# Kernel optimization log

Hardware: AMD Instinct MI355X
Metric: run time of the kernel (lower is better)

Reference implementation:

```python
import jax, jax.numpy as jnp
import numpy as np

B, T, D, H = 2, 2048, 1024, 16
HD = D // H  # head_dim = 64


def setup_inputs() -> dict:
    key = jax.random.key(0)
    k1, k2, k3 = jax.random.split(key, 3)
    s = 0.02
    return {
        "x": jax.random.normal(k1, (B, T, D), dtype=jnp.float32),
        "Wqkv": jax.random.normal(k2, (D, 3 * D), dtype=jnp.float32) * s,
        "bqkv": jnp.zeros((3 * D,), dtype=jnp.float32),
        "Wout": jax.random.normal(k3, (D, D), dtype=jnp.float32) * s,
        "bout": jnp.zeros((D,), dtype=jnp.float32),
    }


def reference(x, Wqkv, bqkv, Wout, bout):
    Bx, Tx, Dx = x.shape
    qkv = x @ Wqkv + bqkv                                  # [B,T,3D]
    qkv = qkv.reshape(Bx, Tx, 3, H, HD)
    q, k, v = (jnp.moveaxis(qkv, 2, 0)[i] for i in range(3))  # each [B,T,H,HD]
    q = q.transpose(0, 2, 1, 3)  # [B,H,T,HD]
    k = k.transpose(0, 2, 1, 3)
    v = v.transpose(0, 2, 1, 3)
    scale = 1.0 / jnp.sqrt(jnp.float32(HD))
    attn = jnp.einsum("bhqd,bhkd->bhqk", q, k) * scale     # [B,H,T,T]
    causal = jnp.tril(jnp.ones((Tx, Tx), dtype=bool))
    attn = jnp.where(causal, attn, -jnp.inf)
    attn = jax.nn.softmax(attn, axis=-1)
    out = jnp.einsum("bhqk,bhkd->bhqd", attn, v)           # [B,H,T,HD]
    out = out.transpose(0, 2, 1, 3).reshape(Bx, Tx, Dx)
    return out @ Wout + bout
```

## Files before the change

kernel.cpp:

```cpp
#include <hip/hip_runtime.h>
#include <hip/hip_bf16.h>
#include <hip/hip_fp16.h>

typedef __attribute__((ext_vector_type(8))) short bf16x8;
typedef __attribute__((ext_vector_type(4))) float f32x4;
typedef unsigned short u16;
typedef unsigned int uint;

#define Bb 2
#define Tt 2048
#define Dd 1024
#define Hh 16

#define EXP2F(x) __builtin_amdgcn_exp2f(x)

__device__ inline u16 f2bf(float f) {
    union { float f; uint u; } v; v.f = f;
    uint r = v.u + 0x7fffu + ((v.u >> 16) & 1u);
    return (u16)(r >> 16);
}
__device__ inline uint fbits(float f) { union { float f; uint u; } v; v.f = f; return v.u; }
__device__ inline u16 f2h(float f) { return __half_as_ushort(__float2half(f)); }
__device__ inline float h2f(u16 u) { return __half2float(__ushort_as_half(u)); }

__device__ inline void glds16(const u16* g, u16* l) {
    __builtin_amdgcn_global_load_lds(
        (const __attribute__((address_space(1))) void*)g,
        (__attribute__((address_space(3))) void*)l,
        16, 0, 0);
}

__global__ __launch_bounds__(256) void cvt_bf16(
    const float* __restrict__ in, u16* __restrict__ out)
{
    const size_t i = ((size_t)blockIdx.x * 256 + threadIdx.x) * 8;
    const float4 a = *(const float4*)&in[i];
    const float4 b = *(const float4*)&in[i + 4];
    uint4 o;
    o.x = (uint)f2bf(a.x) | ((uint)f2bf(a.y) << 16);
    o.y = (uint)f2bf(a.z) | ((uint)f2bf(a.w) << 16);
    o.z = (uint)f2bf(b.x) | ((uint)f2bf(b.y) << 16);
    o.w = (uint)f2bf(b.z) | ((uint)f2bf(b.w) << 16);
    *(uint4*)&out[i] = o;
}

__global__ __launch_bounds__(256) void transpose_cvt(
    const float* __restrict__ W, u16* __restrict__ Wt, int K, int N)
{
    __shared__ float tile[64][65];
    const int k0 = blockIdx.y * 64, n0 = blockIdx.x * 64;
    const int tid = threadIdx.x;
    const int tr = tid >> 4;
    const int tc = (tid & 15) * 4;

    #pragma unroll
    for (int i = 0; i < 4; ++i) {
        const float4 v = *(const float4*)&W[(size_t)(k0 + tr + i * 16) * N + n0 + tc];
        tile[tr + i * 16][tc + 0] = v.x;
        tile[tr + i * 16][tc + 1] = v.y;
        tile[tr + i * 16][tc + 2] = v.z;
        tile[tr + i * 16][tc + 3] = v.w;
    }
    __syncthreads();
    #pragma unroll
    for (int i = 0; i < 4; ++i) {
        ushort4 o;
        o.x = f2bf(tile[tc + 0][tr + i * 16]);
        o.y = f2bf(tile[tc + 1][tr + i * 16]);
        o.z = f2bf(tile[tc + 2][tr + i * 16]);
        o.w = f2bf(tile[tc + 3][tr + i * 16]);
        *(ushort4*)&Wt[(size_t)(n0 + tr + i * 16) * K + k0 + tc] = o;
    }
}

__global__ __launch_bounds__(256) void gemm_qkv(
    const u16* __restrict__ A, const u16* __restrict__ Bt,
    const float* __restrict__ bias, u16* __restrict__ C,
    u16* __restrict__ vg, int M, int N, int K)
{
    __shared__ u16 As[2][128 * 32];
    __shared__ u16 Bs[2][128 * 32];

    const int tid  = threadIdx.x;
    const int lane = tid & 63;
    const int w    = tid >> 6;
    const int wm   = w >> 1, wn = w & 1;
    const int quad = lane >> 4;
    const int m16  = lane & 15;
    const int row0 = blockIdx.y * 128;
    const int col0 = blockIdx.x * 128;

    f32x4 acc[4][4];
    #pragma unroll
    for (int i = 0; i < 4; ++i)
        #pragma unroll
        for (int j = 0; j < 4; ++j) acc[i][j] = (f32x4){0.f, 0.f, 0.f, 0.f};

    const int sr  = tid >> 2, sqs = tid & 3;
    const int sq  = sqs ^ ((sr >> 1) & 3);
    const int ldsw = w * 512;
    const int slot = quad ^ ((m16 >> 1) & 3);

    const int nIter = K >> 5;

    glds16(&A [(size_t)(row0 + sr) * K + sq * 8],       &As[0][ldsw]);
    glds16(&A [(size_t)(row0 + sr + 64) * K + sq * 8],  &As[0][2048 + ldsw]);
    glds16(&Bt[(size_t)(col0 + sr) * K + sq * 8],       &Bs[0][ldsw]);
    glds16(&Bt[(size_t)(col0 + sr + 64) * K + sq * 8],  &Bs[0][2048 + ldsw]);

    for (int it = 0; it < nIter; ++it) {
        const int cb = it & 1;
        __syncthreads();

        if (it + 1 < nIter) {
            const int ko = (it + 1) << 5;
            const int nb = cb ^ 1;
            glds16(&A [(size_t)(row0 + sr) * K + ko + sq * 8],       &As[nb][ldsw]);
            glds16(&A [(size_t)(row0 + sr + 64) * K + ko + sq * 8],  &As[nb][2048 + ldsw]);
            glds16(&Bt[(size_t)(col0 + sr) * K + ko + sq * 8],       &Bs[nb][ldsw]);
            glds16(&Bt[(size_t)(col0 + sr + 64) * K + ko + sq * 8],  &Bs[nb][2048 + ldsw]);
        }

        bf16x8 af[4], bfr[4];
        #pragma unroll
        for (int mt = 0; mt < 4; ++mt)
            af[mt] = *(const bf16x8*)&As[cb][(wm * 64 + mt * 16 + m16) * 32 + slot * 8];
        #pragma unroll
        for (int nt = 0; nt < 4; ++nt)
            bfr[nt] = *(const bf16x8*)&Bs[cb][(wn * 64 + nt * 16 + m16) * 32 + slot * 8];
        #pragma unroll
        for (int mt = 0; mt < 4; ++mt)
            #pragma unroll
            for (int nt = 0; nt < 4; ++nt)
                acc[mt][nt] = __builtin_amdgcn_mfma_f32_16x16x32_bf16(
                    af[mt], bfr[nt], acc[mt][nt], 0, 0, 0);
    }

    #pragma unroll
    for (int mt = 0; mt < 4; ++mt) {
        #pragma unroll
        for (int nt = 0; nt < 4; ++nt) {
            const int row = row0 + wm * 64 + mt * 16 + quad * 4;
            const int col = col0 + wn * 64 + nt * 16 + m16;
            const float bv = bias[col];
            #pragma unroll
            for (int r = 0; r < 4; ++r) {
                const float v = acc[mt][nt][r] + bv;
                if (col0 < 2048) {
                    C[(size_t)(row + r) * 2048 + col] = f2bf(v);
                } else {
                    const int hcol = col - 2048;
                    const int hh = hcol >> 6, dd = hcol & 63;
                    const int bb = (row + r) >> 11, tt = (row + r) & 2047;
                    vg[((size_t)(bb * Hh + hh) * 64 + dd) * Tt + tt] = f2bf(v);
                }
            }
        }
    }
}

__global__ __launch_bounds__(256) void gemm_out(
    const u16* __restrict__ A, const u16* __restrict__ Bt,
    const float* __restrict__ bias, float* __restrict__ C,
    int M, int N, int K)
{
    __shared__ u16 As[2][64 * 32];
    __shared__ u16 Bs[2][128 * 32];

    const int tid  = threadIdx.x;
    const int lane = tid & 63;
    const int w    = tid >> 6;
    const int wm   = w >> 1, wn = w & 1;
    const int quad = lane >> 4;
    const int m16  = lane & 15;
    const int row0 = blockIdx.y * 64;
    const int col0 = blockIdx.x * 128;

    f32x4 acc[2][4];
    #pragma unroll
    for (int i = 0; i < 2; ++i)
        #pragma unroll
        for (int j = 0; j < 4; ++j) acc[i][j] = (f32x4){0.f, 0.f, 0.f, 0.f};

    const int sr  = tid >> 2, sqs = tid & 3;
    const int sq  = sqs ^ ((sr >> 1) & 3);
    const int ldsw = w * 512;
    const int slot = quad ^ ((m16 >> 1) & 3);

    const int nIter = K >> 5;

    glds16(&A [(size_t)(row0 + sr) * K + sq * 8],       &As[0][ldsw]);
    glds16(&Bt[(size_t)(col0 + sr) * K + sq * 8],       &Bs[0][ldsw]);
    glds16(&Bt[(size_t)(col0 + sr + 64) * K + sq * 8],  &Bs[0][2048 + ldsw]);

    for (int it = 0; it < nIter; ++it) {
        const int cb = it & 1;
        __syncthreads();

        if (it + 1 < nIter) {
            const int ko = (it + 1) << 5;
            const int nb = cb ^ 1;
            glds16(&A [(size_t)(row0 + sr) * K + ko + sq * 8],       &As[nb][ldsw]);
            glds16(&Bt[(size_t)(col0 + sr) * K + ko + sq * 8],       &Bs[nb][ldsw]);
            glds16(&Bt[(size_t)(col0 + sr + 64) * K + ko + sq * 8],  &Bs[nb][2048 + ldsw]);
        }

        bf16x8 af[2], bfr[4];
        #pragma unroll
        for (int mt = 0; mt < 2; ++mt)
            af[mt] = *(const bf16x8*)&As[cb][(wm * 32 + mt * 16 + m16) * 32 + slot * 8];
        #pragma unroll
        for (int nt = 0; nt < 4; ++nt)
            bfr[nt] = *(const bf16x8*)&Bs[cb][(wn * 64 + nt * 16 + m16) * 32 + slot * 8];
        #pragma unroll
        for (int mt = 0; mt < 2; ++mt)
            #pragma unroll
            for (int nt = 0; nt < 4; ++nt)
                acc[mt][nt] = __builtin_amdgcn_mfma_f32_16x16x32_bf16(
                    af[mt], bfr[nt], acc[mt][nt], 0, 0, 0);
    }

    #pragma unroll
    for (int mt = 0; mt < 2; ++mt) {
        #pragma unroll
        for (int nt = 0; nt < 4; ++nt) {
            const int row = row0 + wm * 32 + mt * 16 + quad * 4;
            const int col = col0 + wn * 64 + nt * 16 + m16;
            const float bv = bias[col];
            #pragma unroll
            for (int r = 0; r < 4; ++r)
                C[(size_t)(row + r) * N + col] = acc[mt][nt][r] + bv;
        }
    }
}

__global__ __launch_bounds__(256, 4) void attn_split(
    const u16* __restrict__ qkvb, const u16* __restrict__ vglob,
    u16* __restrict__ wsO, float* __restrict__ wsL)
{
    const int hb  = blockIdx.x;
    const int h   = hb & 15, b = hb >> 4;
    const int qt  = 15 - (blockIdx.y >> 2);
    const int quarter = blockIdx.y & 3;
    const int tid = threadIdx.x;
    const int lane = tid & 63, w = tid >> 6;
    const int quad = lane >> 4, m16 = lane & 15;

    __shared__ u16 KV[2][64 * 64];
    __shared__ u16 Pt[128 * 72];

    const int q0 = qt * 128;
    const size_t qkbase = (size_t)(b * Tt) * 2048;
    const size_t vbase  = (size_t)((b * Hh + h) * 64) * Tt;

    const int sr8 = tid >> 3;
    const int sq8 = (tid & 7) ^ (sr8 & 7);
    const int ldsw = w * 512;
    const int slot = quad ^ (m16 & 7);

    bf16x8 qb[2][2];
    #pragma unroll
    for (int nt = 0; nt < 2; ++nt)
        #pragma unroll
        for (int ks = 0; ks < 2; ++ks)
            qb[nt][ks] = *(const bf16x8*)&qkvb[
                qkbase + (size_t)(q0 + w * 32 + nt * 16 + m16) * 2048
                + h * 64 + ks * 32 + quad * 8];

    f32x4 o[4][2];
    #pragma unroll
    for (int ct = 0; ct < 4; ++ct)
        #pragma unroll
        for (int nt = 0; nt < 2; ++nt) o[ct][nt] = (f32x4){0.f, 0.f, 0.f, 0.f};
    float ls[2] = {0.f, 0.f};
    const float sc2 = 0.125f * 1.4426950408889634f;

    const int ntiles = 2 * qt + 2;
    for (int kt = quarter; kt < ntiles; kt += 4) {
        const int k0 = kt * 64;
        __syncthreads();
        #pragma unroll
        for (int j = 0; j < 2; ++j) {
            const int row = j * 32 + sr8;
            glds16(&qkvb[qkbase + (size_t)(k0 + row) * 2048 + 1024 + h * 64 + sq8 * 8],
                   &KV[0][j * 2048 + ldsw]);
            glds16(&vglob[vbase + (size_t)row * Tt + k0 + sq8 * 8],
                   &KV[1][j * 2048 + ldsw]);
        }
        __syncthreads();

        if (k0 <= q0 + w * 32 + 31) {
            const u16* Ks = KV[0];
            const u16* Vt = KV[1];

            bf16x8 ak[4][2];
            #pragma unroll
            for (int mt = 0; mt < 4; ++mt) {
                const int ro = (mt * 16 + m16) * 64;
                ak[mt][0] = *(const bf16x8*)&Ks[ro + slot * 8];
                ak[mt][1] = *(const bf16x8*)&Ks[ro + (slot ^ 4) * 8];
            }
            f32x4 s[4][2];
            #pragma unroll
            for (int mt = 0; mt < 4; ++mt)
                #pragma unroll
                for (int nt = 0; nt < 2; ++nt) {
                    f32x4 a = (f32x4){0.f, 0.f, 0.f, 0.f};
                    a = __builtin_amdgcn_mfma_f32_16x16x32_bf16(ak[mt][0], qb[nt][0], a, 0, 0, 0);
                    a = __builtin_amdgcn_mfma_f32_16x16x32_bf16(ak[mt][1], qb[nt][1], a, 0, 0, 0);
                    s[mt][nt] = a;
                }

            const int qi0 = q0 + w * 32 + m16;
            const bool diag = (k0 + 63 > q0 + w * 32);
            #pragma unroll
            for (int mt = 0; mt < 4; ++mt)
                #pragma unroll
                for (int nt = 0; nt < 2; ++nt) {
                    float p[4];
                    const int kb = k0 + mt * 16 + quad * 4;
                    #pragma unroll
                    for (int r = 0; r < 4; ++r) {
                        float t = __builtin_fmaf(s[mt][nt][r], sc2, -8.0f);
                        if (diag) t = (kb + r <= qi0 + nt * 16) ? t : -1000.0f;
                        p[r] = EXP2F(t);
                    }
                    ls[nt] += (p[0] + p[1]) + (p[2] + p[3]);
                    uint2 pk;
                    pk.x = (fbits(p[0]) >> 16) | (fbits(p[1]) & 0xffff0000u);
                    pk.y = (fbits(p[2]) >> 16) | (fbits(p[3]) & 0xffff0000u);
                    *(uint2*)&Pt[(w * 32 + nt * 16 + m16) * 72 + mt * 16 + quad * 4] = pk;
                }

            bf16x8 av[4][2], pb[2][2];
            #pragma unroll
            for (int ct = 0; ct < 4; ++ct) {
                const int ro = (ct * 16 + m16) * 64;
                av[ct][0] = *(const bf16x8*)&Vt[ro + slot * 8];
                av[ct][1] = *(const bf16x8*)&Vt[ro + (slot ^ 4) * 8];
            }
            #pragma unroll
            for (int nt = 0; nt < 2; ++nt)
                #pragma unroll
                for (int ks = 0; ks < 2; ++ks)
                    pb[nt][ks] = *(const bf16x8*)&Pt[(w * 32 + nt * 16 + m16) * 72 + ks * 32 + quad * 8];
            #pragma unroll
            for (int ct = 0; ct < 4; ++ct)
                #pragma unroll
                for (int nt = 0; nt < 2; ++nt) {
                    o[ct][nt] = __builtin_amdgcn_mfma_f32_16x16x32_bf16(av[ct][0], pb[nt][0], o[ct][nt], 0, 0, 0);
                    o[ct][nt] = __builtin_amdgcn_mfma_f32_16x16x32_bf16(av[ct][1], pb[nt][1], o[ct][nt], 0, 0, 0);
                }
        }
    }

    #pragma unroll
    for (int nt = 0; nt < 2; ++nt) {
        ls[nt] += __shfl_xor(ls[nt], 16);
        ls[nt] += __shfl_xor(ls[nt], 32);
    }
    const int qrow = b * Tt + q0 + w * 32 + m16;
    if (quad == 0) {
        wsL[(quarter * Hh + h) * 4096 + qrow]      = ls[0];
        wsL[(quarter * Hh + h) * 4096 + qrow + 16] = ls[1];
    }
    #pragma unroll
    for (int ct = 0; ct < 4; ++ct)
        #pragma unroll
        for (int nt = 0; nt < 2; ++nt) {
            ushort4 pk;
            pk.x = f2h(o[ct][nt][0]);
            pk.y = f2h(o[ct][nt][1]);
            pk.z = f2h(o[ct][nt][2]);
            pk.w = f2h(o[ct][nt][3]);
            *(ushort4*)&wsO[((size_t)quarter * 4096 + qrow + nt * 16) * 1024
                            + h * 64 + ct * 16 + quad * 4] = pk;
        }
}

__global__ __launch_bounds__(256) void combine(
    const u16* __restrict__ wsO, const float* __restrict__ wsL,
    u16* __restrict__ attb)
{
    const int gi  = (blockIdx.x * 256 + threadIdx.x) * 8;
    const int row = gi >> 10;
    const int h   = (gi & 1023) >> 6;
    float lsum = 0.f;
    #pragma unroll
    for (int p = 0; p < 4; ++p)
        lsum += wsL[(p * Hh + h) * 4096 + row];
    const float il = 1.0f / lsum;

    uint4 part[4];
    #pragma unroll
    for (int p = 0; p < 4; ++p)
        part[p] = *(const uint4*)&wsO[(size_t)p * 4096 * 1024 + gi];
    const uint* pw = (const uint*)part;

    uint ow[4];
    #pragma unroll
    for (int i = 0; i < 4; ++i) {
        float r0 = 0.f, r1 = 0.f;
        #pragma unroll
        for (int p = 0; p < 4; ++p) {
            const uint v = pw[p * 4 + i];
            r0 += h2f((u16)(v & 0xffff));
            r1 += h2f((u16)(v >> 16));
        }
        ow[i] = (uint)f2bf(r0 * il) | ((uint)f2bf(r1 * il) << 16);
    }
    uint4 o4; o4.x = ow[0]; o4.y = ow[1]; o4.z = ow[2]; o4.w = ow[3];
    *(uint4*)&attb[gi] = o4;
}

extern "C" void kernel_launch(void* const* d_in, const int* in_sizes, int n_in,
                              void* d_out, int out_size, void* d_ws, size_t ws_size,
                              hipStream_t stream) {
    const float* x    = (const float*)d_in[0];
    const float* Wqkv = (const float*)d_in[1];
    const float* bqkv = (const float*)d_in[2];
    const float* Wout = (const float*)d_in[3];
    const float* bout = (const float*)d_in[4];
    float* out = (float*)d_out;

    u16*   xb    = (u16*)d_ws;
    u16*   WqT   = xb    + (size_t)4096 * 1024;
    u16*   WoT   = WqT   + (size_t)3072 * 1024;
    u16*   qkvb  = WoT   + (size_t)1024 * 1024;
    u16*   vglob = qkvb  + (size_t)4096 * 2048;
    u16*   wsO   = vglob + (size_t)4096 * 1024;
    float* wsL   = (float*)(wsO + (size_t)4 * 4096 * 1024);
    u16*   attb  = xb;

    cvt_bf16<<<dim3((4096 * 1024) / 8 / 256), dim3(256), 0, stream>>>(x, xb);
    transpose_cvt<<<dim3(3072 / 64, 1024 / 64), dim3(256), 0, stream>>>(Wqkv, WqT, 1024, 3072);
    transpose_cvt<<<dim3(1024 / 64, 1024 / 64), dim3(256), 0, stream>>>(Wout, WoT, 1024, 1024);

    gemm_qkv<<<dim3(3072 / 128, 4096 / 128), dim3(256), 0, stream>>>(
        xb, WqT, bqkv, qkvb, vglob, 4096, 3072, 1024);

    attn_split<<<dim3(Hh * Bb, 64), dim3(256), 0, stream>>>(qkvb, vglob, wsO, wsL);

    combine<<<dim3((4096 * 1024) / 8 / 256), dim3(256), 0, stream>>>(wsO, wsL, attb);

    gemm_out<<<dim3(1024 / 128, 4096 / 64), dim3(256), 0, stream>>>(
        attb, WoT, bout, out, 4096, 1024, 1024);
}
```

Measured before the change: 190.5 us.

## Fuse split-attention combine into output GEMM A-loading and merge prep kernels

Merges the x conversion and both weight transpose-conversions into one prep kernel, removing two launches. Drops the separate combine kernel: the output GEMM now reads the four fp16 partial outputs and normalizers directly, reduces and normalizes them in registers, and writes bf16 tiles into shared memory. This removes the attb round-trip through global memory and one launch. The cost is that each GEMM column block (8 of them) re-reads and recombines the partials, and the A path now uses synchronous register loads instead of async global-to-LDS copies.

Measured after the change: 204.5 us. +7.4%, slower.

```diff
diff --git a/kernel.cpp b/kernel.cpp
--- a/kernel.cpp
+++ b/kernel.cpp
@@ -30,29 +30,43 @@
         16, 0, 0);
 }
 
-__global__ __launch_bounds__(256) void cvt_bf16(
-    const float* __restrict__ in, u16* __restrict__ out)
-{
-    const size_t i = ((size_t)blockIdx.x * 256 + threadIdx.x) * 8;
-    const float4 a = *(const float4*)&in[i];
-    const float4 b = *(const float4*)&in[i + 4];
-    uint4 o;
-    o.x = (uint)f2bf(a.x) | ((uint)f2bf(a.y) << 16);
-    o.y = (uint)f2bf(a.z) | ((uint)f2bf(a.w) << 16);
-    o.z = (uint)f2bf(b.x) | ((uint)f2bf(b.y) << 16);
-    o.w = (uint)f2bf(b.z) | ((uint)f2bf(b.w) << 16);
-    *(uint4*)&out[i] = o;
-}
-
-__global__ __launch_bounds__(256) void transpose_cvt(
-    const float* __restrict__ W, u16* __restrict__ Wt, int K, int N)
+__global__ __launch_bounds__(256) void prep(
+    const float* __restrict__ x, const float* __restrict__ Wqkv,
+    const float* __restrict__ Wout, u16* __restrict__ xb,
+    u16* __restrict__ WqT, u16* __restrict__ WoT)
 {
     __shared__ float tile[64][65];
-    const int k0 = blockIdx.y * 64, n0 = blockIdx.x * 64;
+    const int bid = blockIdx.x;
     const int tid = threadIdx.x;
+
+    if (bid < 2048) {
+        const size_t i = ((size_t)bid * 256 + tid) * 8;
+        const float4 a = *(const float4*)&x[i];
+        const float4 b = *(const float4*)&x[i + 4];
+        uint4 o;
+        o.x = (uint)f2bf(a.x) | ((uint)f2bf(a.y) << 16);
+        o.y = (uint)f2bf(a.z) | ((uint)f2bf(a.w) << 16);
+        o.z = (uint)f2bf(b.x) | ((uint)f2bf(b.y) << 16);
+        o.w = (uint)f2bf(b.z) | ((uint)f2bf(b.w) << 16);
+        *(uint4*)&xb[i] = o;
+        return;
+    }
+
+    const float* W;
+    u16* Wt;
+    int k0, n0, K, N;
+    if (bid < 2816) {
+        const int tb = bid - 2048;
+        W = Wqkv; Wt = WqT; K = 1024; N = 3072;
+        n0 = (tb % 48) * 64; k0 = (tb / 48) * 64;
+    } else {
+        const int tb = bid - 2816;
+        W = Wout; Wt = WoT; K = 1024; N = 1024;
+        n0 = (tb % 16) * 64; k0 = (tb / 16) * 64;
+    }
+
     const int tr = tid >> 4;
     const int tc = (tid & 15) * 4;
-
     #pragma unroll
     for (int i = 0; i < 4; ++i) {
         const float4 v = *(const float4*)&W[(size_t)(k0 + tr + i * 16) * N + n0 + tc];
@@ -155,81 +169,6 @@
                     vg[((size_t)(bb * Hh + hh) * 64 + dd) * Tt + tt] = f2bf(v);
                 }
             }
-        }
-    }
-}
-
-__global__ __launch_bounds__(256) void gemm_out(
-    const u16* __restrict__ A, const u16* __restrict__ Bt,
-    const float* __restrict__ bias, float* __restrict__ C,
-    int M, int N, int K)
-{
-    __shared__ u16 As[2][64 * 32];
-    __shared__ u16 Bs[2][128 * 32];
-
-    const int tid  = threadIdx.x;
-    const int lane = tid & 63;
-    const int w    = tid >> 6;
-    const int wm   = w >> 1, wn = w & 1;
-    const int quad = lane >> 4;
-    const int m16  = lane & 15;
-    const int row0 = blockIdx.y * 64;
-    const int col0 = blockIdx.x * 128;
-
-    f32x4 acc[2][4];
-    #pragma unroll
-    for (int i = 0; i < 2; ++i)
-        #pragma unroll
-        for (int j = 0; j < 4; ++j) acc[i][j] = (f32x4){0.f, 0.f, 0.f, 0.f};
-
-    const int sr  = tid >> 2, sqs = tid & 3;
-    const int sq  = sqs ^ ((sr >> 1) & 3);
-    const int ldsw = w * 512;
-    const int slot = quad ^ ((m16 >> 1) & 3);
-
-    const int nIter = K >> 5;
-
-    glds16(&A [(size_t)(row0 + sr) * K + sq * 8],       &As[0][ldsw]);
-    glds16(&Bt[(size_t)(col0 + sr) * K + sq * 8],       &Bs[0][ldsw]);
-    glds16(&Bt[(size_t)(col0 + sr + 64) * K + sq * 8],  &Bs[0][2048 + ldsw]);
-
-    for (int it = 0; it < nIter; ++it) {
-        const int cb = it & 1;
-        __syncthreads();
-
-        if (it + 1 < nIter) {
-            const int ko = (it + 1) << 5;
-            const int nb = cb ^ 1;
-            glds16(&A [(size_t)(row0 + sr) * K + ko + sq * 8],       &As[nb][ldsw]);
-            glds16(&Bt[(size_t)(col0 + sr) * K + ko + sq * 8],       &Bs[nb][ldsw]);
-            glds16(&Bt[(size_t)(col0 + sr + 64) * K + ko + sq * 8],  &Bs[nb][2048 + ldsw]);
-        }
-
-        bf16x8 af[2], bfr[4];
-        #pragma unroll
-        for (int mt = 0; mt < 2; ++mt)
-            af[mt] = *(const bf16x8*)&As[cb][(wm * 32 + mt * 16 + m16) * 32 + slot * 8];
-        #pragma unroll
-        for (int nt = 0; nt < 4; ++nt)
-            bfr[nt] = *(const bf16x8*)&Bs[cb][(wn * 64 + nt * 16 + m16) * 32 + slot * 8];
-        #pragma unroll
-        for (int mt = 0; mt < 2; ++mt)
-            #pragma unroll
-            for (int nt = 0; nt < 4; ++nt)
-                acc[mt][nt] = __builtin_amdgcn_mfma_f32_16x16x32_bf16(
-                    af[mt], bfr[nt], acc[mt][nt], 0, 0, 0);
-    }
-
-    #pragma unroll
-    for (int mt = 0; mt < 2; ++mt) {
-        #pragma unroll
-        for (int nt = 0; nt < 4; ++nt) {
-            const int row = row0 + wm * 32 + mt * 16 + quad * 4;
-            const int col = col0 + wn * 64 + nt * 16 + m16;
-            const float bv = bias[col];
-            #pragma unroll
-            for (int r = 0; r < 4; ++r)
-                C[(size_t)(row + r) * N + col] = acc[mt][nt][r] + bv;
         }
     }
 }
@@ -378,39 +317,120 @@
         }
 }
 
-__global__ __launch_bounds__(256) void combine(
+__global__ __launch_bounds__(256) void gemm_out_fused(
     const u16* __restrict__ wsO, const float* __restrict__ wsL,
-    u16* __restrict__ attb)
+    const u16* __restrict__ Bt, const float* __restrict__ bias,
+    float* __restrict__ C, int M, int N, int K)
 {
-    const int gi  = (blockIdx.x * 256 + threadIdx.x) * 8;
-    const int row = gi >> 10;
-    const int h   = (gi & 1023) >> 6;
-    float lsum = 0.f;
-    #pragma unroll
-    for (int p = 0; p < 4; ++p)
-        lsum += wsL[(p * Hh + h) * 4096 + row];
-    const float il = 1.0f / lsum;
+    __shared__ u16 As[2][64 * 32];
+    __shared__ u16 Bs[2][128 * 32];
+
+    const int tid  = threadIdx.x;
+    const int lane = tid & 63;
+    const int w    = tid >> 6;
+    const int wm   = w >> 1, wn = w & 1;
+    const int quad = lane >> 4;
+    const int m16  = lane & 15;
+    const int row0 = blockIdx.y * 64;
+    const int col0 = blockIdx.x * 128;
+
+    f32x4 acc[2][4];
+    #pragma unroll
+    for (int i = 0; i < 2; ++i)
+        #pragma unroll
+        for (int j = 0; j < 4; ++j) acc[i][j] = (f32x4){0.f, 0.f, 0.f, 0.f};
+
+    const int sr  = tid >> 2, sqs = tid & 3;
+    const int sq  = sqs ^ ((sr >> 1) & 3);
+    const int ldsw = w * 512;
+    const int slot = quad ^ ((m16 >> 1) & 3);
+    const int arow = row0 + sr;
+
+    const int nIter = K >> 5;
 
     uint4 part[4];
-    #pragma unroll
-    for (int p = 0; p < 4; ++p)
-        part[p] = *(const uint4*)&wsO[(size_t)p * 4096 * 1024 + gi];
-    const uint* pw = (const uint*)part;
-
-    uint ow[4];
-    #pragma unroll
-    for (int i = 0; i < 4; ++i) {
-        float r0 = 0.f, r1 = 0.f;
+    #define LOADA(ko)                                                          \
+        _Pragma("unroll")                                                      \
+        for (int p = 0; p < 4; ++p)                                            \
+            part[p] = *(const uint4*)&wsO[((size_t)p * 4096 + arow) * 1024 +   \
+                                          (ko) + sq * 8];
+    auto combineA = [&](int ko, int buf) {
+        const int h = ko >> 6;
+        float lsv = 0.f;
+        #pragma unroll
+        for (int p = 0; p < 4; ++p)
+            lsv += wsL[(size_t)(p * Hh + h) * 4096 + arow];
+        const float il = 1.0f / lsv;
+        uint pw[16];
         #pragma unroll
         for (int p = 0; p < 4; ++p) {
-            const uint v = pw[p * 4 + i];
-            r0 += h2f((u16)(v & 0xffff));
-            r1 += h2f((u16)(v >> 16));
-        }
-        ow[i] = (uint)f2bf(r0 * il) | ((uint)f2bf(r1 * il) << 16);
-    }
-    uint4 o4; o4.x = ow[0]; o4.y = ow[1]; o4.z = ow[2]; o4.w = ow[3];
-    *(uint4*)&attb[gi] = o4;
+            pw[p * 4 + 0] = part[p].x; pw[p * 4 + 1] = part[p].y;
+            pw[p * 4 + 2] = part[p].z; pw[p * 4 + 3] = part[p].w;
+        }
+        uint ow[4];
+        #pragma unroll
+        for (int i = 0; i < 4; ++i) {
+            float r0 = 0.f, r1 = 0.f;
+            #pragma unroll
+            for (int p = 0; p < 4; ++p) {
+                const uint v = pw[p * 4 + i];
+                r0 += h2f((u16)(v & 0xffff));
+                r1 += h2f((u16)(v >> 16));
+            }
+            ow[i] = (uint)f2bf(r0 * il) | ((uint)f2bf(r1 * il) << 16);
+        }
+        uint4 o4; o4.x = ow[0]; o4.y = ow[1]; o4.z = ow[2]; o4.w = ow[3];
+        *(uint4*)&As[buf][sr * 32 + sqs * 8] = o4;
+    };
+
+    LOADA(sq * 0);
+    glds16(&Bt[(size_t)(col0 + sr) * K + sq * 8],       &Bs[0][ldsw]);
+    glds16(&Bt[(size_t)(col0 + sr + 64) * K + sq * 8],  &Bs[0][2048 + ldsw]);
+    combineA(0, 0);
+
+    for (int it = 0; it < nIter; ++it) {
+        const int cb = it & 1;
+        __syncthreads();
+
+        const int nb = cb ^ 1;
+        const int ko = (it + 1) << 5;
+        if (it + 1 < nIter) {
+            LOADA(ko);
+            glds16(&Bt[(size_t)(col0 + sr) * K + ko + sq * 8],       &Bs[nb][ldsw]);
+            glds16(&Bt[(size_t)(col0 + sr + 64) * K + ko + sq * 8],  &Bs[nb][2048 + ldsw]);
+        }
+
+        bf16x8 af[2], bfr[4];
+        #pragma unroll
+        for (int mt = 0; mt < 2; ++mt)
+            af[mt] = *(const bf16x8*)&As[cb][(wm * 32 + mt * 16 + m16) * 32 + slot * 8];
+        #pragma unroll
+        for (int nt = 0; nt < 4; ++nt)
+            bfr[nt] = *(const bf16x8*)&Bs[cb][(wn * 64 + nt * 16 + m16) * 32 + slot * 8];
+        #pragma unroll
+        for (int mt = 0; mt < 2; ++mt)
+            #pragma unroll
+            for (int nt = 0; nt < 4; ++nt)
+                acc[mt][nt] = __builtin_amdgcn_mfma_f32_16x16x32_bf16(
+                    af[mt], bfr[nt], acc[mt][nt], 0, 0, 0);
+
+        if (it + 1 < nIter)
+            combineA(ko, nb);
+    }
+
+    #pragma unroll
+    for (int mt = 0; mt < 2; ++mt) {
+        #pragma unroll
+        for (int nt = 0; nt < 4; ++nt) {
+            const int row = row0 + wm * 32 + mt * 16 + quad * 4;
+            const int col = col0 + wn * 64 + nt * 16 + m16;
+            const float bv = bias[col];
+            #pragma unroll
+            for (int r = 0; r < 4; ++r)
+                C[(size_t)(row + r) * N + col] = acc[mt][nt][r] + bv;
+        }
+    }
+    #undef LOADA
 }
 
 extern "C" void kernel_launch(void* const* d_in, const int* in_sizes, int n_in,
@@ -430,19 +450,14 @@
     u16*   vglob = qkvb  + (size_t)4096 * 2048;
     u16*   wsO   = vglob + (size_t)4096 * 1024;
     float* wsL   = (float*)(wsO + (size_t)4 * 4096 * 1024);
-    u16*   attb  = xb;
-
-    cvt_bf16<<<dim3((4096 * 1024) / 8 / 256), dim3(256), 0, stream>>>(x, xb);
-    transpose_cvt<<<dim3(3072 / 64, 1024 / 64), dim3(256), 0, stream>>>(Wqkv, WqT, 1024, 3072);
-    transpose_cvt<<<dim3(1024 / 64, 1024 / 64), dim3(256), 0, stream>>>(Wout, WoT, 1024, 1024);
+
+    prep<<<dim3(3072), dim3(256), 0, stream>>>(x, Wqkv, Wout, xb, WqT, WoT);
 
     gemm_qkv<<<dim3(3072 / 128, 4096 / 128), dim3(256), 0, stream>>>(
         xb, WqT, bqkv, qkvb, vglob, 4096, 3072, 1024);
 
     attn_split<<<dim3(Hh * Bb, 64), dim3(256), 0, stream>>>(qkvb, vglob, wsO, wsL);
 
-    combine<<<dim3((4096 * 1024) / 8 / 256), dim3(256), 0, stream>>>(wsO, wsL, attb);
-
-    gemm_out<<<dim3(1024 / 128, 4096 / 64), dim3(256), 0, stream>>>(
-        attb, WoT, bout, out, 4096, 1024, 1024);
-}
+    gemm_out_fused<<<dim3(1024 / 128, 4096 / 64), dim3(256), 0, stream>>>(
+        wsO, wsL, WoT, bout, out, 4096, 1024, 1024);
+}
```
